# Kernel optimization log

Hardware: AMD Instinct MI355X
Metric: run time of the kernel (lower is better)

## Reference

```python
import jax, jax.numpy as jnp
import numpy as np

B, L, D_IN, H = 64, 512, 1024, 1024

def setup_inputs() -> dict:
    key = jax.random.key(0)
    k1, k2, k3 = jax.random.split(key, 3)
    x = jax.random.normal(k1, (B, L, D_IN), dtype=jnp.float32)
    # nn.Linear(input_sz + hidden_dim, 4*hidden_dim): weight [4H, H + D_IN], bias [4H]
    # concat order in forward is (hidden_state, input_at_t)
    W = jax.random.normal(k2, (4 * H, H + D_IN), dtype=jnp.float32) * 0.02
    b = jax.random.normal(k3, (4 * H,), dtype=jnp.float32) * 0.02
    return {"x": x, "W": W, "b": b}

def reference(x, W, b):
    Bsz = x.shape[0]
    Hd = W.shape[0] // 4
    # split weight into hidden part and input part (concat order: [h, x_t])
    Wh = W[:, :Hd]          # [4H, H]
    Wx = W[:, Hd:]          # [4H, D_IN]
    # precompute input projections for all timesteps: [B, L, 4H]
    x_proj = jnp.einsum('bld,gd->blg', x, Wx) + b
    h0 = jnp.zeros((Bsz, Hd), dtype=x.dtype)
    c0 = jnp.zeros((Bsz, Hd), dtype=x.dtype)

    def step(carry, xp_t):
        h, c = carry
        gates = xp_t + h @ Wh.T                     # [B, 4H]
        f_l, i_l, g_l, o_l = jnp.split(gates, 4, axis=-1)
        f = jax.nn.sigmoid(f_l)
        i = jax.nn.sigmoid(i_l)
        g = jnp.tanh(g_l)
        o = jax.nn.sigmoid(o_l)
        c_new = f * c + i * g
        h_new = o * jnp.tanh(c_new)
        return (h_new, c_new), h_new

    (h_fin, c_fin), hs = jax.lax.scan(step, (h0, c0), jnp.swapaxes(x_proj, 0, 1))
    outputs = jnp.swapaxes(hs, 0, 1)  # [B, L, H]
    return outputs, (h_fin, c_fin)
```

## Files before the change

kernel.cpp:

```cpp
#include <hip/hip_runtime.h>
#include <hip/hip_bf16.h>
#include <stdint.h>

#define B_SZ   64
#define L_SEQ  512
#define DIN    1024
#define HDIM   1024
#define G4     4096
#define OUT_HFIN 33554432L
#define OUT_CFIN 33619968L

typedef float  f32x4 __attribute__((ext_vector_type(4)));
typedef short  s16x8 __attribute__((ext_vector_type(8)));
typedef unsigned short u16;
typedef unsigned long long u64;

#define OFF_XBF   0ULL
#define OFF_WX    67108864ULL
#define OFF_WH    75497472ULL
#define OFF_XPROJ 83886080ULL
#define OFF_HBUF  352321536ULL
#define OFF_FLG   352583680ULL

static __device__ __forceinline__ u16 f2bf(float f) {
    __hip_bfloat16 h = __float2bfloat16(f);
    return *reinterpret_cast<u16*>(&h);
}
static __device__ __forceinline__ float bf2f(u16 u) {
    union { uint32_t i; float f; } v;
    v.i = ((uint32_t)u) << 16;
    return v.f;
}
static __device__ __forceinline__ float fsigmoid(float x) {
    return __builtin_amdgcn_rcpf(1.0f + __expf(-x));
}
static __device__ __forceinline__ float ftanh(float x) {
    return 1.0f - 2.0f * __builtin_amdgcn_rcpf(1.0f + __expf(2.0f * x));
}

__global__ void prep_kernel(const float* __restrict__ x, const float* __restrict__ W,
                            u16* __restrict__ xbf, u16* __restrict__ wx,
                            u16* __restrict__ wh, int* __restrict__ flg) {
    long tid = (long)blockIdx.x * blockDim.x + threadIdx.x;
    long stride = (long)gridDim.x * blockDim.x;
    const long NX4 = 33554432 / 4;
    for (long i = tid; i < NX4; i += stride) {
        float4 v = ((const float4*)x)[i];
        ushort4 o;
        o.x = f2bf(v.x); o.y = f2bf(v.y); o.z = f2bf(v.z); o.w = f2bf(v.w);
        ((ushort4*)xbf)[i] = o;
    }
    const long NW4 = 8388608 / 4;
    for (long i = tid; i < NW4; i += stride) {
        float4 v = ((const float4*)W)[i];
        long f = i * 4;
        long n = f >> 11;
        long c = f & 2047;
        ushort4 o;
        o.x = f2bf(v.x); o.y = f2bf(v.y); o.z = f2bf(v.z); o.w = f2bf(v.w);
        u16* dst = (c < 1024) ? &wh[n * 1024 + c] : &wx[n * 1024 + (c - 1024)];
        *(ushort4*)dst = o;
    }
    if (blockIdx.x == 0 && threadIdx.x < 256) flg[threadIdx.x] = 0;
}

__global__ __launch_bounds__(256) void xproj_gemm(const u16* __restrict__ xbf,
                                                  const u16* __restrict__ wxbf,
                                                  const float* __restrict__ bias,
                                                  u16* __restrict__ xproj) {
    __shared__ u16 As[128 * 32];
    __shared__ u16 Bs[128 * 32];
    const int tid  = threadIdx.x;
    const int lane = tid & 63;
    const int w    = tid >> 6;
    const int wm   = w >> 1, wn = w & 1;
    const int l15  = lane & 15, quad = lane >> 4;
    const int m0 = blockIdx.y * 128;
    const int n0 = blockIdx.x * 128;

    const int rowA = tid >> 2,          colA = (tid & 3) * 8;
    const int rowB = (tid + 256) >> 2,  colB = ((tid + 256) & 3) * 8;

    f32x4 acc[4][4];
#pragma unroll
    for (int i = 0; i < 4; ++i)
#pragma unroll
        for (int j = 0; j < 4; ++j) acc[i][j] = 0.0f;

    s16x8 a0 = *(const s16x8*)&xbf [(long)(m0 + rowA) * 1024 + colA];
    s16x8 a1 = *(const s16x8*)&xbf [(long)(m0 + rowB) * 1024 + colB];
    s16x8 b0 = *(const s16x8*)&wxbf[(long)(n0 + rowA) * 1024 + colA];
    s16x8 b1 = *(const s16x8*)&wxbf[(long)(n0 + rowB) * 1024 + colB];

    for (int kt = 0; kt < 32; ++kt) {
        *(s16x8*)&As[rowA * 32 + colA] = a0;
        *(s16x8*)&As[rowB * 32 + colB] = a1;
        *(s16x8*)&Bs[rowA * 32 + colA] = b0;
        *(s16x8*)&Bs[rowB * 32 + colB] = b1;
        __syncthreads();
        if (kt < 31) {
            const int k0 = (kt + 1) * 32;
            a0 = *(const s16x8*)&xbf [(long)(m0 + rowA) * 1024 + k0 + colA];
            a1 = *(const s16x8*)&xbf [(long)(m0 + rowB) * 1024 + k0 + colB];
            b0 = *(const s16x8*)&wxbf[(long)(n0 + rowA) * 1024 + k0 + colA];
            b1 = *(const s16x8*)&wxbf[(long)(n0 + rowB) * 1024 + k0 + colB];
        }
        s16x8 af[4], bfr[4];
#pragma unroll
        for (int mt = 0; mt < 4; ++mt)
            af[mt] = *(const s16x8*)&As[(wm * 64 + mt * 16 + l15) * 32 + quad * 8];
#pragma unroll
        for (int nt = 0; nt < 4; ++nt)
            bfr[nt] = *(const s16x8*)&Bs[(wn * 64 + nt * 16 + l15) * 32 + quad * 8];
#pragma unroll
        for (int mt = 0; mt < 4; ++mt)
#pragma unroll
            for (int nt = 0; nt < 4; ++nt)
                acc[mt][nt] = __builtin_amdgcn_mfma_f32_16x16x32_bf16(af[mt], bfr[nt], acc[mt][nt], 0, 0, 0);
        __syncthreads();
    }
#pragma unroll
    for (int nt = 0; nt < 4; ++nt) {
        int n = n0 + wn * 64 + nt * 16 + l15;
        float bv = bias[n];
#pragma unroll
        for (int mt = 0; mt < 4; ++mt) {
            int mbase = m0 + wm * 64 + mt * 16 + quad * 4;
#pragma unroll
            for (int r = 0; r < 4; ++r)
                xproj[(long)(mbase + r) * 4096 + n] = f2bf(acc[mt][nt][r] + bv);
        }
    }
}

__global__ __launch_bounds__(256, 1) void lstm_rec(const u16* __restrict__ whbf,
                                                   const u16* __restrict__ xproj,
                                                   u16* __restrict__ hbuf,
                                                   float* __restrict__ out,
                                                   int* __restrict__ flg) {
    __shared__ u16   h_s[16 * 1032];
    __shared__ float part[4][16][16][4];
    __shared__ u16   how[4][4][16];

    const int tid  = threadIdx.x;
    const int w    = tid >> 6;
    const int lane = tid & 63;
    const int l15  = lane & 15, quad = lane >> 4;
    const int g    = blockIdx.x & 3;
    const int jc   = blockIdx.x >> 2;
    const int bbase = g * 16;
    const int crow = 4 * w + (lane >> 4);
    const int ccol = l15;
    int* fl = flg + g * 64;

    s16x8 bfrag[4][8];
#pragma unroll
    for (int gate = 0; gate < 4; ++gate) {
        const long nrow = (long)gate * 1024 + jc * 16 + l15;
#pragma unroll
        for (int kc = 0; kc < 8; ++kc)
            bfrag[gate][kc] = *(const s16x8*)&whbf[nrow * 1024 + w * 256 + kc * 32 + quad * 8];
    }

    float c_reg = 0.0f;
    u64* hb64[2] = { (u64*)hbuf, (u64*)(hbuf + 65536) };

    const u16* xpcell = xproj + (long)(bbase + crow) * 512 * 4096 + jc * 16 + ccol;
    float xp[4];
#pragma unroll
    for (int gate = 0; gate < 4; ++gate)
        xp[gate] = bf2f(xpcell[(long)gate * 1024]);

    for (int t = 0; t < 512; ++t) {
        if (t == 0) {
            u64 z = 0;
#pragma unroll
            for (int it = 0; it < 16; ++it) {
                int s = tid + it * 256;
                *(u64*)&h_s[(s >> 8) * 1032 + (s & 255) * 4] = z;
            }
        } else {
            int v = __hip_atomic_load(&fl[lane], __ATOMIC_RELAXED, __HIP_MEMORY_SCOPE_AGENT);
            while (__ballot(v < t) != 0ULL) {
                __builtin_amdgcn_s_sleep(1);
                v = __hip_atomic_load(&fl[lane], __ATOMIC_RELAXED, __HIP_MEMORY_SCOPE_AGENT);
            }
            const u64* hsrc = hb64[(t + 1) & 1];
            u64 tmp[16];
#pragma unroll
            for (int it = 0; it < 16; ++it) {
                int s = tid + it * 256;
                tmp[it] = __hip_atomic_load(&hsrc[(bbase + (s >> 8)) * 256 + (s & 255)],
                                            __ATOMIC_RELAXED, __HIP_MEMORY_SCOPE_AGENT);
            }
#pragma unroll
            for (int it = 0; it < 16; ++it) {
                int s = tid + it * 256;
                *(u64*)&h_s[(s >> 8) * 1032 + (s & 255) * 4] = tmp[it];
            }
        }
        __syncthreads();

        f32x4 acc[4];
#pragma unroll
        for (int gate = 0; gate < 4; ++gate) acc[gate] = 0.0f;
#pragma unroll
        for (int kc = 0; kc < 8; ++kc) {
            s16x8 a = *(const s16x8*)&h_s[l15 * 1032 + w * 256 + kc * 32 + quad * 8];
            acc[0] = __builtin_amdgcn_mfma_f32_16x16x32_bf16(a, bfrag[0][kc], acc[0], 0, 0, 0);
            acc[1] = __builtin_amdgcn_mfma_f32_16x16x32_bf16(a, bfrag[1][kc], acc[1], 0, 0, 0);
            acc[2] = __builtin_amdgcn_mfma_f32_16x16x32_bf16(a, bfrag[2][kc], acc[2], 0, 0, 0);
            acc[3] = __builtin_amdgcn_mfma_f32_16x16x32_bf16(a, bfrag[3][kc], acc[3], 0, 0, 0);
        }
#pragma unroll
        for (int gate = 0; gate < 4; ++gate)
#pragma unroll
            for (int r = 0; r < 4; ++r)
                part[gate][quad * 4 + r][l15][w] = acc[gate][r];
        __syncthreads();

        float gv[4];
#pragma unroll
        for (int gate = 0; gate < 4; ++gate) {
            f32x4 p = *(const f32x4*)&part[gate][crow][ccol][0];
            gv[gate] = ((p[0] + p[1]) + (p[2] + p[3])) + xp[gate];
        }
        float fv = fsigmoid(gv[0]);
        float iv = fsigmoid(gv[1]);
        float gg = ftanh   (gv[2]);
        float ov = fsigmoid(gv[3]);
        c_reg = fv * c_reg + iv * gg;
        float h = ov * ftanh(c_reg);

        long bg = bbase + crow;
        long j  = jc * 16 + ccol;
        out[(bg * 512 + t) * 1024 + j] = h;
        how[w][lane >> 4][ccol] = f2bf(h);
        if (t == 511) {
            out[OUT_HFIN + bg * 1024 + j] = h;
            out[OUT_CFIN + bg * 1024 + j] = c_reg;
        }

        if (t < 511) {
            if (lane < 16) {
                int prow = 4 * w + (lane >> 2);
                int c4   = (lane & 3) * 4;
                u64 v = *(const u64*)&how[w][lane >> 2][c4];
                __hip_atomic_store(&hb64[t & 1][((long)(bbase + prow) * 1024 + jc * 16 + c4) >> 2],
                                   v, __ATOMIC_RELAXED, __HIP_MEMORY_SCOPE_AGENT);
            }
            __asm__ volatile("s_waitcnt vmcnt(0)" ::: "memory");
            __syncthreads();
            if (tid == 0)
                __hip_atomic_store(&fl[jc], t + 1, __ATOMIC_RELAXED, __HIP_MEMORY_SCOPE_AGENT);
#pragma unroll
            for (int gate = 0; gate < 4; ++gate)
                xp[gate] = bf2f(xpcell[((long)t + 1) * 4096 + (long)gate * 1024]);
        }
    }
}

extern "C" void kernel_launch(void* const* d_in, const int* in_sizes, int n_in,
                              void* d_out, int out_size, void* d_ws, size_t ws_size,
                              hipStream_t stream) {
    const float* x    = (const float*)d_in[0];
    const float* W    = (const float*)d_in[1];
    const float* bias = (const float*)d_in[2];
    float* out = (float*)d_out;
    char*  ws  = (char*)d_ws;

    u16* xbf   = (u16*)(ws + OFF_XBF);
    u16* wx    = (u16*)(ws + OFF_WX);
    u16* wh    = (u16*)(ws + OFF_WH);
    u16* xproj = (u16*)(ws + OFF_XPROJ);
    u16* hbuf  = (u16*)(ws + OFF_HBUF);
    int* flg   = (int*)(ws + OFF_FLG);

    hipLaunchKernelGGL(prep_kernel, dim3(2048), dim3(256), 0, stream, x, W, xbf, wx, wh, flg);
    hipLaunchKernelGGL(xproj_gemm, dim3(32, 256), dim3(256), 0, stream, xbf, wx, bias, xproj);
    hipLaunchKernelGGL(lstm_rec, dim3(256), dim3(256), 0, stream, wh, xproj, hbuf, out, flg);
}
```

Baseline: 2.197 ms.

## Direct-to-LDS double-buffered GEMM loads and register-resident hidden state in recurrence

The input-projection GEMM now uses global_load_lds into double-buffered shared tiles, prefetching the next K tile while MFMAs run on the current one. The recurrent kernel no longer stages h through shared memory with a block barrier. Each wave loads only the K-slice of h it needs straight into MFMA operand registers and polls only the producer flags for its slice. The hidden-state publish and flag store now come before the output write, which shortens the critical path between timesteps, though the polling is narrower per wave and the GEMM uses more LDS.

After: 2.643 ms. 20.3% more time.

```diff
diff --git a/kernel.cpp b/kernel.cpp
--- a/kernel.cpp
+++ b/kernel.cpp
@@ -36,6 +36,10 @@
 }
 static __device__ __forceinline__ float ftanh(float x) {
     return 1.0f - 2.0f * __builtin_amdgcn_rcpf(1.0f + __expf(2.0f * x));
+}
+static __device__ __forceinline__ void gload_lds16(const u16* g, u16* l) {
+    __builtin_amdgcn_global_load_lds((const __attribute__((address_space(1))) void*)g,
+                                     (__attribute__((address_space(3))) void*)l, 16, 0, 0);
 }
 
 __global__ void prep_kernel(const float* __restrict__ x, const float* __restrict__ W,
@@ -68,8 +72,8 @@
                                                   const u16* __restrict__ wxbf,
                                                   const float* __restrict__ bias,
                                                   u16* __restrict__ xproj) {
-    __shared__ u16 As[128 * 32];
-    __shared__ u16 Bs[128 * 32];
+    __shared__ u16 As[2][128 * 32];
+    __shared__ u16 Bs[2][128 * 32];
     const int tid  = threadIdx.x;
     const int lane = tid & 63;
     const int w    = tid >> 6;
@@ -78,8 +82,8 @@
     const int m0 = blockIdx.y * 128;
     const int n0 = blockIdx.x * 128;
 
-    const int rowA = tid >> 2,          colA = (tid & 3) * 8;
-    const int rowB = (tid + 256) >> 2,  colB = ((tid + 256) & 3) * 8;
+    const u16* ga = xbf  + (long)(m0 + (tid >> 2)) * 1024 + (tid & 3) * 8;
+    const u16* gb = wxbf + (long)(n0 + (tid >> 2)) * 1024 + (tid & 3) * 8;
 
     f32x4 acc[4][4];
 #pragma unroll
@@ -87,38 +91,38 @@
 #pragma unroll
         for (int j = 0; j < 4; ++j) acc[i][j] = 0.0f;
 
-    s16x8 a0 = *(const s16x8*)&xbf [(long)(m0 + rowA) * 1024 + colA];
-    s16x8 a1 = *(const s16x8*)&xbf [(long)(m0 + rowB) * 1024 + colB];
-    s16x8 b0 = *(const s16x8*)&wxbf[(long)(n0 + rowA) * 1024 + colA];
-    s16x8 b1 = *(const s16x8*)&wxbf[(long)(n0 + rowB) * 1024 + colB];
+#define STAGE(buf, k0)                                                    \
+    do {                                                                  \
+        gload_lds16(ga + (k0),         &As[buf][w * 512]);                \
+        gload_lds16(ga + 65536 + (k0), &As[buf][2048 + w * 512]);         \
+        gload_lds16(gb + (k0),         &Bs[buf][w * 512]);                \
+        gload_lds16(gb + 65536 + (k0), &Bs[buf][2048 + w * 512]);         \
+    } while (0)
+
+    STAGE(0, 0);
+    __syncthreads();
 
     for (int kt = 0; kt < 32; ++kt) {
-        *(s16x8*)&As[rowA * 32 + colA] = a0;
-        *(s16x8*)&As[rowB * 32 + colB] = a1;
-        *(s16x8*)&Bs[rowA * 32 + colA] = b0;
-        *(s16x8*)&Bs[rowB * 32 + colB] = b1;
-        __syncthreads();
-        if (kt < 31) {
-            const int k0 = (kt + 1) * 32;
-            a0 = *(const s16x8*)&xbf [(long)(m0 + rowA) * 1024 + k0 + colA];
-            a1 = *(const s16x8*)&xbf [(long)(m0 + rowB) * 1024 + k0 + colB];
-            b0 = *(const s16x8*)&wxbf[(long)(n0 + rowA) * 1024 + k0 + colA];
-            b1 = *(const s16x8*)&wxbf[(long)(n0 + rowB) * 1024 + k0 + colB];
-        }
+        const int cur = kt & 1;
+        if (kt < 31) STAGE(cur ^ 1, (kt + 1) * 32);
+
         s16x8 af[4], bfr[4];
 #pragma unroll
         for (int mt = 0; mt < 4; ++mt)
-            af[mt] = *(const s16x8*)&As[(wm * 64 + mt * 16 + l15) * 32 + quad * 8];
+            af[mt] = *(const s16x8*)&As[cur][(wm * 64 + mt * 16 + l15) * 32 + quad * 8];
 #pragma unroll
         for (int nt = 0; nt < 4; ++nt)
-            bfr[nt] = *(const s16x8*)&Bs[(wn * 64 + nt * 16 + l15) * 32 + quad * 8];
+            bfr[nt] = *(const s16x8*)&Bs[cur][(wn * 64 + nt * 16 + l15) * 32 + quad * 8];
 #pragma unroll
         for (int mt = 0; mt < 4; ++mt)
 #pragma unroll
             for (int nt = 0; nt < 4; ++nt)
                 acc[mt][nt] = __builtin_amdgcn_mfma_f32_16x16x32_bf16(af[mt], bfr[nt], acc[mt][nt], 0, 0, 0);
+
         __syncthreads();
     }
+#undef STAGE
+
 #pragma unroll
     for (int nt = 0; nt < 4; ++nt) {
         int n = n0 + wn * 64 + nt * 16 + l15;
@@ -138,7 +142,6 @@
                                                    u16* __restrict__ hbuf,
                                                    float* __restrict__ out,
                                                    int* __restrict__ flg) {
-    __shared__ u16   h_s[16 * 1032];
     __shared__ float part[4][16][16][4];
     __shared__ u16   how[4][4][16];
 
@@ -151,7 +154,8 @@
     const int bbase = g * 16;
     const int crow = 4 * w + (lane >> 4);
     const int ccol = l15;
-    int* fl = flg + g * 64;
+    int* fl   = flg + g * 64;
+    int* myfl = fl + w * 16 + (lane & 15);
 
     s16x8 bfrag[4][8];
 #pragma unroll
@@ -164,6 +168,7 @@
 
     float c_reg = 0.0f;
     u64* hb64[2] = { (u64*)hbuf, (u64*)(hbuf + 65536) };
+    const long rbase = (((long)(bbase + l15)) * 1024 + w * 256 + quad * 8) >> 2;
 
     const u16* xpcell = xproj + (long)(bbase + crow) * 512 * 4096 + jc * 16 + ccol;
     float xp[4];
@@ -172,41 +177,32 @@
         xp[gate] = bf2f(xpcell[(long)gate * 1024]);
 
     for (int t = 0; t < 512; ++t) {
+        union AF { u64 d[2]; s16x8 v; } af[8];
         if (t == 0) {
-            u64 z = 0;
-#pragma unroll
-            for (int it = 0; it < 16; ++it) {
-                int s = tid + it * 256;
-                *(u64*)&h_s[(s >> 8) * 1032 + (s & 255) * 4] = z;
-            }
+#pragma unroll
+            for (int kc = 0; kc < 8; ++kc) { af[kc].d[0] = 0ULL; af[kc].d[1] = 0ULL; }
         } else {
-            int v = __hip_atomic_load(&fl[lane], __ATOMIC_RELAXED, __HIP_MEMORY_SCOPE_AGENT);
-            while (__ballot(v < t) != 0ULL) {
+            int pv = __hip_atomic_load(myfl, __ATOMIC_RELAXED, __HIP_MEMORY_SCOPE_AGENT);
+            while (__ballot(pv < t) != 0ULL) {
                 __builtin_amdgcn_s_sleep(1);
-                v = __hip_atomic_load(&fl[lane], __ATOMIC_RELAXED, __HIP_MEMORY_SCOPE_AGENT);
+                pv = __hip_atomic_load(myfl, __ATOMIC_RELAXED, __HIP_MEMORY_SCOPE_AGENT);
             }
             const u64* hsrc = hb64[(t + 1) & 1];
-            u64 tmp[16];
-#pragma unroll
-            for (int it = 0; it < 16; ++it) {
-                int s = tid + it * 256;
-                tmp[it] = __hip_atomic_load(&hsrc[(bbase + (s >> 8)) * 256 + (s & 255)],
-                                            __ATOMIC_RELAXED, __HIP_MEMORY_SCOPE_AGENT);
+#pragma unroll
+            for (int kc = 0; kc < 8; ++kc) {
+                af[kc].d[0] = __hip_atomic_load(&hsrc[rbase + kc * 8],
+                                                __ATOMIC_RELAXED, __HIP_MEMORY_SCOPE_AGENT);
+                af[kc].d[1] = __hip_atomic_load(&hsrc[rbase + kc * 8 + 1],
+                                                __ATOMIC_RELAXED, __HIP_MEMORY_SCOPE_AGENT);
             }
-#pragma unroll
-            for (int it = 0; it < 16; ++it) {
-                int s = tid + it * 256;
-                *(u64*)&h_s[(s >> 8) * 1032 + (s & 255) * 4] = tmp[it];
-            }
-        }
-        __syncthreads();
+        }
 
         f32x4 acc[4];
 #pragma unroll
         for (int gate = 0; gate < 4; ++gate) acc[gate] = 0.0f;
 #pragma unroll
         for (int kc = 0; kc < 8; ++kc) {
-            s16x8 a = *(const s16x8*)&h_s[l15 * 1032 + w * 256 + kc * 32 + quad * 8];
+            s16x8 a = af[kc].v;
             acc[0] = __builtin_amdgcn_mfma_f32_16x16x32_bf16(a, bfrag[0][kc], acc[0], 0, 0, 0);
             acc[1] = __builtin_amdgcn_mfma_f32_16x16x32_bf16(a, bfrag[1][kc], acc[1], 0, 0, 0);
             acc[2] = __builtin_amdgcn_mfma_f32_16x16x32_bf16(a, bfrag[2][kc], acc[2], 0, 0, 0);
@@ -232,27 +228,28 @@
         c_reg = fv * c_reg + iv * gg;
         float h = ov * ftanh(c_reg);
 
-        long bg = bbase + crow;
-        long j  = jc * 16 + ccol;
-        out[(bg * 512 + t) * 1024 + j] = h;
-        how[w][lane >> 4][ccol] = f2bf(h);
-        if (t == 511) {
-            out[OUT_HFIN + bg * 1024 + j] = h;
-            out[OUT_CFIN + bg * 1024 + j] = c_reg;
-        }
-
         if (t < 511) {
+            how[w][lane >> 4][ccol] = f2bf(h);
             if (lane < 16) {
                 int prow = 4 * w + (lane >> 2);
                 int c4   = (lane & 3) * 4;
-                u64 v = *(const u64*)&how[w][lane >> 2][c4];
+                u64 hv = *(const u64*)&how[w][lane >> 2][c4];
                 __hip_atomic_store(&hb64[t & 1][((long)(bbase + prow) * 1024 + jc * 16 + c4) >> 2],
-                                   v, __ATOMIC_RELAXED, __HIP_MEMORY_SCOPE_AGENT);
+                                   hv, __ATOMIC_RELAXED, __HIP_MEMORY_SCOPE_AGENT);
             }
             __asm__ volatile("s_waitcnt vmcnt(0)" ::: "memory");
             __syncthreads();
             if (tid == 0)
                 __hip_atomic_store(&fl[jc], t + 1, __ATOMIC_RELAXED, __HIP_MEMORY_SCOPE_AGENT);
+        }
+
+        long bg = bbase + crow;
+        long j  = jc * 16 + ccol;
+        out[(bg * 512 + t) * 1024 + j] = h;
+        if (t == 511) {
+            out[OUT_HFIN + bg * 1024 + j] = h;
+            out[OUT_CFIN + bg * 1024 + j] = c_reg;
+        } else {
 #pragma unroll
             for (int gate = 0; gate < 4; ++gate)
                 xp[gate] = bf2f(xpcell[((long)t + 1) * 4096 + (long)gate * 1024]);
```
